# Kernel tuning notes

Hardware: AMD Instinct MI355X
Metric: run time of the kernel (lower is better)

## Reference

```python
import jax, jax.numpy as jnp
import numpy as np

B, S, D, H, O, E, K = 4, 2048, 1024, 2048, 1024, 8, 2

def setup_inputs() -> dict:
    key = jax.random.key(0)
    ks = jax.random.split(key, 8)
    x = jax.random.normal(ks[0], (B, S, D), dtype=jnp.float32)
    # kaiming-uniform-ish scale for weights, zero biases (as in _init_w)
    gate_w = jax.random.uniform(ks[1], (E, D), dtype=jnp.float32, minval=-1, maxval=1) * np.sqrt(6.0 / D)
    gate_b = jnp.zeros((E,), dtype=jnp.float32)
    w1 = jax.random.uniform(ks[2], (E, D, H), dtype=jnp.float32, minval=-1, maxval=1) * np.sqrt(6.0 / D)
    b1 = jnp.zeros((E, H), dtype=jnp.float32)
    w2 = jax.random.uniform(ks[3], (E, H, O), dtype=jnp.float32, minval=-1, maxval=1) * np.sqrt(6.0 / H)
    b2 = jnp.zeros((E, O), dtype=jnp.float32)
    return {"x": x, "gate_w": gate_w, "gate_b": gate_b, "w1": w1, "b1": b1, "w2": w2, "b2": b2}

def reference(x, gate_w, gate_b, w1, b1, w2, b2):
    # gate: softmax over experts, then top-k (k=2)
    logits = jnp.einsum('bsd,ed->bse', x, gate_w) + gate_b          # [B,S,E]
    probs = jax.nn.softmax(logits, axis=-1)
    topk_vals, topk_idx = jax.lax.top_k(probs, K)                    # [B,S,K]
    # dense all-expert MLPs (Linear-ReLU-Linear), dropout = 0
    h = jax.nn.relu(jnp.einsum('bsd,edh->bseh', x, w1) + b1)         # [B,S,E,H]
    expert_out = jnp.einsum('bseh,eho->bseo', h, w2) + b2            # [B,S,E,O]
    # gather top-k experts and combine with gate weights
    sel = jnp.take_along_axis(expert_out, topk_idx[..., None], axis=2)  # [B,S,K,O]
    return jnp.sum(sel * topk_vals[..., None], axis=2)               # [B,S,O]
```

## Files before the change

kernel.cpp:

```cpp
#include <hip/hip_runtime.h>

#define T_TOKENS 8192
#define D_DIM 1024
#define H_DIM 2048
#define O_DIM 1024
#define E_NUM 8
#define NPAIR 16384
#define GY_MAX 136

typedef unsigned short u16;
typedef __bf16 bf16x8 __attribute__((ext_vector_type(8)));
typedef float f32x4 __attribute__((ext_vector_type(4)));

#define VMCNT(n) asm volatile("s_waitcnt vmcnt(" #n ")" ::: "memory")

__device__ __forceinline__ void barsync() {
  asm volatile("" ::: "memory");
  __builtin_amdgcn_s_barrier();
  __builtin_amdgcn_sched_barrier(0);
}

__device__ inline u16 f2bf(float f) {
  union { float f; unsigned u; } v; v.f = f;
  unsigned r = v.u + 0x7FFFu + ((v.u >> 16) & 1u);
  return (u16)(r >> 16);
}

__device__ __forceinline__ void gload16(const u16* g, u16* l) {
  __builtin_amdgcn_global_load_lds((const __attribute__((address_space(1))) void*)g,
                                   (__attribute__((address_space(3))) void*)l, 16, 0, 0);
}

__global__ void transpose_cvt_kernel(const float* __restrict__ w, u16* __restrict__ wt,
                                     int R, int C) {
  __shared__ float tile[32][33];
  int e = blockIdx.z;
  int c0 = blockIdx.x * 32, r0 = blockIdx.y * 32;
  const float* wp = w + (size_t)e * R * C;
  u16* wtp = wt + (size_t)e * R * C;
  int tx = threadIdx.x, ty = threadIdx.y;
  #pragma unroll
  for (int j = 0; j < 32; j += 8)
    tile[ty + j][tx] = wp[(size_t)(r0 + ty + j) * C + c0 + tx];
  __syncthreads();
  #pragma unroll
  for (int j = 0; j < 32; j += 8)
    wtp[(size_t)(c0 + ty + j) * R + r0 + tx] = f2bf(tile[tx][ty + j]);
}

__global__ void gate_kernel(const float* __restrict__ x, const float* __restrict__ gw,
                            const float* __restrict__ gb, int* __restrict__ topk_idx,
                            float* __restrict__ topk_val, u16* __restrict__ xb) {
  int t = blockIdx.x * 4 + (threadIdx.x >> 6);
  int lane = threadIdx.x & 63;
  const float4* xr4 = (const float4*)(x + (size_t)t * D_DIM);
  const float4* gw4 = (const float4*)gw;
  u16* xbr = xb + (size_t)t * D_DIM;
  float acc[E_NUM];
  #pragma unroll
  for (int e = 0; e < E_NUM; e++) acc[e] = 0.f;
  #pragma unroll
  for (int it = 0; it < D_DIM / 256; ++it) {
    float4 xv = xr4[it * 64 + lane];
    ushort4 o;
    o.x = f2bf(xv.x); o.y = f2bf(xv.y); o.z = f2bf(xv.z); o.w = f2bf(xv.w);
    *(ushort4*)(xbr + (it * 64 + lane) * 4) = o;
    #pragma unroll
    for (int e = 0; e < E_NUM; e++) {
      float4 wv = gw4[e * (D_DIM / 4) + it * 64 + lane];
      acc[e] += xv.x * wv.x + xv.y * wv.y + xv.z * wv.z + xv.w * wv.w;
    }
  }
  #pragma unroll
  for (int e = 0; e < E_NUM; e++) {
    #pragma unroll
    for (int o = 32; o > 0; o >>= 1) acc[e] += __shfl_down(acc[e], o);
  }
  if (lane == 0) {
    float l[E_NUM], mx = -1e30f;
    #pragma unroll
    for (int e = 0; e < E_NUM; e++) { l[e] = acc[e] + gb[e]; mx = fmaxf(mx, l[e]); }
    float p[E_NUM], s = 0.f;
    #pragma unroll
    for (int e = 0; e < E_NUM; e++) { p[e] = expf(l[e] - mx); s += p[e]; }
    float inv = 1.f / s;
    int i1 = 0;
    #pragma unroll
    for (int e = 1; e < E_NUM; e++) if (p[e] > p[i1]) i1 = e;
    int i2 = (i1 == 0) ? 1 : 0;
    #pragma unroll
    for (int e = 0; e < E_NUM; e++) if (e != i1 && e != i2 && p[e] > p[i2]) i2 = e;
    topk_idx[t * 2] = i1;     topk_idx[t * 2 + 1] = i2;
    topk_val[t * 2] = p[i1] * inv; topk_val[t * 2 + 1] = p[i2] * inv;
  }
}

__global__ void histscan_kernel(const int* __restrict__ topk_idx,
                                int* __restrict__ counts, int* __restrict__ eoff,
                                int* __restrict__ nblk, int* __restrict__ tbl_e,
                                int* __restrict__ tbl_m0) {
  __shared__ int wh[4][E_NUM];
  int tid = threadIdx.x;
  int lane = tid & 63, wave = tid >> 6;
  int myc = 0;
  for (int i = tid; i < NPAIR; i += 256) {
    int e = topk_idx[i];
    #pragma unroll
    for (int ee = 0; ee < E_NUM; ee++) {
      unsigned long long m = __ballot(e == ee);
      if (lane == ee) myc += __popcll(m);
    }
  }
  if (lane < E_NUM) wh[wave][lane] = myc;
  __syncthreads();
  if (tid == 0) {
    int s = 0, cl[E_NUM];
    for (int e = 0; e < E_NUM; e++) {
      int c = wh[0][e] + wh[1][e] + wh[2][e] + wh[3][e];
      counts[e] = c;
      cl[e] = c;
      eoff[e] = s;
      s += c;
    }
    eoff[E_NUM] = s;
    int nb = 0;
    for (int e = 0; e < E_NUM; e++)
      for (int m0 = 0; m0 < cl[e]; m0 += 128) { tbl_e[nb] = e; tbl_m0[nb] = m0; nb++; }
    nblk[0] = nb;
  }
}

__global__ void scatter_kernel(const int* __restrict__ topk_idx, const float* __restrict__ topk_val,
                               const int* __restrict__ eoff, int* __restrict__ cursor_pad,
                               int* __restrict__ pair_token, float* __restrict__ pair_gate) {
  __shared__ int lhist[E_NUM];
  __shared__ int lbase[E_NUM];
  int tid = threadIdx.x;
  int t = blockIdx.x * 256 + tid;
  if (tid < E_NUM) lhist[tid] = 0;
  __syncthreads();
  int e0 = topk_idx[t * 2], e1 = topk_idx[t * 2 + 1];
  int r0 = atomicAdd(&lhist[e0], 1);
  int r1 = atomicAdd(&lhist[e1], 1);
  __syncthreads();
  if (tid < E_NUM) lbase[tid] = eoff[tid] + atomicAdd(&cursor_pad[tid * 32], lhist[tid]);
  __syncthreads();
  int p0 = lbase[e0] + r0;
  int p1 = lbase[e1] + r1;
  pair_token[p0] = t; pair_gate[p0] = topk_val[t * 2];
  pair_token[p1] = t; pair_gate[p1] = topk_val[t * 2 + 1];
}


#define GEMM_DECLS                                                             \
  __shared__ __align__(16) u16 As0[4096], Bs0[4096], As1[4096], Bs1[4096],     \
      As2[4096], Bs2[4096];                                                    \
  const int tid = threadIdx.x;                                                 \
  const int wid = tid >> 6;                                                    \
  const int lane = tid & 63;                                                   \
  const int wm = (wid & 1) * 64;                                               \
  const int wn = (wid >> 1) * 64;                                              \
  const int lrow = lane & 15;                                                  \
  const int quad = lane >> 4;                                                  \
  f32x4 acc[4][4] = {};                                                        \
  auto STAGE = [&](u16* Ab, u16* Bb, int k0) {                                 \
    _Pragma("unroll")                                                          \
    for (int j = 0; j < 2; j++) {                                              \
      gload16(aptrA[j] + k0, Ab + (wid * 16 + j * 8) * 64);                    \
      gload16(bptrB[j] + k0, Bb + (wid * 16 + j * 8) * 64);                    \
    }                                                                          \
  };                                                                           \
  auto COMPUTE = [&](const u16* Ab, const u16* Bb) {                           \
    bf16x8 af[4], bfr[4];                                                      \
    _Pragma("unroll")                                                          \
    for (int i = 0; i < 4; i++) {                                              \
      int r = wm + i * 16 + lrow;                                              \
      int p = r >> 1;                                                          \
      int s = (((r & 1) << 2) | quad) ^ (p & 7);                               \
      af[i] = *(const bf16x8*)&Ab[p * 64 + s * 8];                             \
    }                                                                          \
    _Pragma("unroll")                                                          \
    for (int j = 0; j < 4; j++) {                                              \
      int r = wn + j * 16 + lrow;                                              \
      int p = r >> 1;                                                          \
      int s = (((r & 1) << 2) | quad) ^ (p & 7);                               \
      bfr[j] = *(const bf16x8*)&Bb[p * 64 + s * 8];                            \
    }                                                                          \
    __builtin_amdgcn_s_setprio(1);                                             \
    _Pragma("unroll")                                                          \
    for (int i = 0; i < 4; i++)                                                \
      _Pragma("unroll")                                                        \
      for (int j = 0; j < 4; j++)                                              \
        acc[i][j] = __builtin_amdgcn_mfma_f32_16x16x32_bf16(af[i], bfr[j],     \
                                                            acc[i][j], 0, 0, 0);\
    __builtin_amdgcn_s_setprio(0);                                             \
  }

__global__ __launch_bounds__(256, 3) void gemm1_kernel(
    const u16* __restrict__ xb, const u16* __restrict__ w1t, const float* __restrict__ b1,
    const int* __restrict__ pair_token, const int* __restrict__ eoff,
    const int* __restrict__ ecnt, const int* __restrict__ nblk,
    const int* __restrict__ tbl_e, const int* __restrict__ tbl_m0,
    u16* __restrict__ hbuf) {
  int lin = blockIdx.y * 16 + blockIdx.x;
  int swz = (lin & 7) * (16 * GY_MAX / 8) + (lin >> 3);
  const int bx = swz & 15;
  const int yb = swz >> 4;
  if (yb >= nblk[0]) return;
  const int e = tbl_e[yb];
  const int m0t = tbl_m0[yb];
  const int ne = ecnt[e];
  const int off = eoff[e];
  const int n0 = bx * 128;

  const u16* aptrA[2]; const u16* bptrB[2];
  {
    const int wid_ = threadIdx.x >> 6, lane_ = threadIdx.x & 63;
    #pragma unroll
    for (int j = 0; j < 2; j++) {
      int p = wid_ * 16 + j * 8 + (lane_ >> 3);
      int u = (lane_ & 7) ^ (p & 7);
      int r = 2 * p + (u >> 2);
      int c = u & 3;
      int gm = m0t + r;
      int tok = (gm < ne) ? pair_token[off + gm] : 0;
      aptrA[j] = xb + (size_t)tok * D_DIM + c * 8;
      bptrB[j] = w1t + ((size_t)e * H_DIM + (n0 + r)) * D_DIM + c * 8;
    }
  }

  GEMM_DECLS;

  STAGE(As0, Bs0, 0); STAGE(As1, Bs1, 32); STAGE(As2, Bs2, 64);
  #pragma unroll 1
  for (int t = 0; t <= 32 - 6; t += 3) {
    VMCNT(8); barsync(); COMPUTE(As0, Bs0); barsync(); STAGE(As0, Bs0, (t + 3) * 32);
    VMCNT(8); barsync(); COMPUTE(As1, Bs1); barsync(); STAGE(As1, Bs1, (t + 4) * 32);
    VMCNT(8); barsync(); COMPUTE(As2, Bs2); barsync(); STAGE(As2, Bs2, (t + 5) * 32);
  }
  VMCNT(8); barsync(); COMPUTE(As0, Bs0); barsync(); STAGE(As0, Bs0, 30 * 32);
  VMCNT(8); barsync(); COMPUTE(As1, Bs1); barsync(); STAGE(As1, Bs1, 31 * 32);
  VMCNT(8); barsync(); COMPUTE(As2, Bs2);
  VMCNT(4); barsync(); COMPUTE(As0, Bs0);
  VMCNT(0); barsync(); COMPUTE(As1, Bs1);

  #pragma unroll
  for (int i = 0; i < 4; i++) {
    #pragma unroll
    for (int r = 0; r < 4; r++) {
      int m = wm + i * 16 + quad * 4 + r;
      int gm = m0t + m;
      if (gm >= ne) continue;
      size_t rowbase = (size_t)(off + gm) * H_DIM;
      #pragma unroll
      for (int j = 0; j < 4; j++) {
        int n = n0 + wn + j * 16 + lrow;
        float v = acc[i][j][r] + b1[e * H_DIM + n];
        v = v > 0.f ? v : 0.f;
        hbuf[rowbase + n] = f2bf(v);
      }
    }
  }
}

__global__ __launch_bounds__(256, 3) void gemm2_kernel(
    const u16* __restrict__ hbuf, const u16* __restrict__ w2t, const float* __restrict__ b2,
    const int* __restrict__ pair_token, const float* __restrict__ pair_gate,
    const int* __restrict__ eoff, const int* __restrict__ ecnt,
    const int* __restrict__ nblk, const int* __restrict__ tbl_e,
    const int* __restrict__ tbl_m0, float* __restrict__ out) {
  int lin = blockIdx.y * 8 + blockIdx.x;
  int swz = (lin & 7) * (8 * GY_MAX / 8) + (lin >> 3);
  const int bx = swz & 7;
  const int yb = swz >> 3;
  if (yb >= nblk[0]) return;
  const int e = tbl_e[yb];
  const int m0t = tbl_m0[yb];
  const int ne = ecnt[e];
  const int off = eoff[e];
  const int n0 = bx * 128;

  const u16* aptrA[2]; const u16* bptrB[2];
  {
    const int wid_ = threadIdx.x >> 6, lane_ = threadIdx.x & 63;
    #pragma unroll
    for (int j = 0; j < 2; j++) {
      int p = wid_ * 16 + j * 8 + (lane_ >> 3);
      int u = (lane_ & 7) ^ (p & 7);
      int r = 2 * p + (u >> 2);
      int c = u & 3;
      aptrA[j] = hbuf + (size_t)(off + m0t + r) * H_DIM + c * 8;
      bptrB[j] = w2t + ((size_t)e * O_DIM + (n0 + r)) * H_DIM + c * 8;
    }
  }

  GEMM_DECLS;

  STAGE(As0, Bs0, 0); STAGE(As1, Bs1, 32); STAGE(As2, Bs2, 64);
  #pragma unroll 1
  for (int t = 0; t <= 64 - 6; t += 3) {
    VMCNT(8); barsync(); COMPUTE(As0, Bs0); barsync(); STAGE(As0, Bs0, (t + 3) * 32);
    VMCNT(8); barsync(); COMPUTE(As1, Bs1); barsync(); STAGE(As1, Bs1, (t + 4) * 32);
    VMCNT(8); barsync(); COMPUTE(As2, Bs2); barsync(); STAGE(As2, Bs2, (t + 5) * 32);
  }
  VMCNT(8); barsync(); COMPUTE(As0, Bs0); barsync(); STAGE(As0, Bs0, 63 * 32);
  VMCNT(8); barsync(); COMPUTE(As1, Bs1);
  VMCNT(4); barsync(); COMPUTE(As2, Bs2);
  VMCNT(0); barsync(); COMPUTE(As0, Bs0);

  #pragma unroll
  for (int i = 0; i < 4; i++) {
    #pragma unroll
    for (int r = 0; r < 4; r++) {
      int m = wm + i * 16 + quad * 4 + r;
      int gm = m0t + m;
      if (gm >= ne) continue;
      int pair = off + gm;
      int tok = pair_token[pair];
      float g = pair_gate[pair];
      #pragma unroll
      for (int j = 0; j < 4; j++) {
        int n = n0 + wn + j * 16 + lrow;
        float v = (acc[i][j][r] + b2[e * O_DIM + n]) * g;
        atomicAdd(&out[(size_t)tok * O_DIM + n], v);
      }
    }
  }
}

extern "C" void kernel_launch(void* const* d_in, const int* in_sizes, int n_in,
                              void* d_out, int out_size, void* d_ws, size_t ws_size,
                              hipStream_t stream) {
  const float* x  = (const float*)d_in[0];
  const float* gw = (const float*)d_in[1];
  const float* gb = (const float*)d_in[2];
  const float* w1 = (const float*)d_in[3];
  const float* b1 = (const float*)d_in[4];
  const float* w2 = (const float*)d_in[5];
  const float* b2 = (const float*)d_in[6];
  float* out = (float*)d_out;

  char* ws = (char*)d_ws;
  size_t off = 0;
  auto take = [&](size_t bytes) -> char* {
    char* p = ws + off;
    off = (off + bytes + 255) & ~(size_t)255;
    return p;
  };
  int*   meta       = (int*)take(4096);
  int*   cursor_pad = meta;
  int*   counts     = meta + 256;
  int*   eoff       = meta + 264;
  int*   nblk       = meta + 273;
  int*   tbl_e      = meta + 274;
  int*   tbl_m0     = meta + 410;
  int*   topk_idx   = (int*)take((size_t)T_TOKENS * 2 * 4);
  float* topk_val   = (float*)take((size_t)T_TOKENS * 2 * 4);
  int*   pair_token = (int*)take((size_t)(NPAIR + 256) * 4);
  float* pair_gate  = (float*)take((size_t)(NPAIR + 256) * 4);
  u16*   xb         = (u16*)take((size_t)T_TOKENS * D_DIM * 2);
  u16*   w1t        = (u16*)take((size_t)E_NUM * D_DIM * H_DIM * 2);
  u16*   w2t        = (u16*)take((size_t)E_NUM * H_DIM * O_DIM * 2);
  u16*   hbuf       = (u16*)take((size_t)(NPAIR + 128) * H_DIM * 2);

  hipMemsetAsync(meta, 0, 4096, stream);
  hipMemsetAsync(out, 0, (size_t)T_TOKENS * O_DIM * 4, stream);

  transpose_cvt_kernel<<<dim3(H_DIM / 32, D_DIM / 32, E_NUM), dim3(32, 8), 0, stream>>>(w1, w1t, D_DIM, H_DIM);
  transpose_cvt_kernel<<<dim3(O_DIM / 32, H_DIM / 32, E_NUM), dim3(32, 8), 0, stream>>>(w2, w2t, H_DIM, O_DIM);
  gate_kernel<<<T_TOKENS / 4, 256, 0, stream>>>(x, gw, gb, topk_idx, topk_val, xb);
  histscan_kernel<<<1, 256, 0, stream>>>(topk_idx, counts, eoff, nblk, tbl_e, tbl_m0);
  scatter_kernel<<<T_TOKENS / 256, 256, 0, stream>>>(topk_idx, topk_val, eoff, cursor_pad, pair_token, pair_gate);
  gemm1_kernel<<<dim3(16, GY_MAX), 256, 0, stream>>>(xb, w1t, b1, pair_token, eoff, counts, nblk, tbl_e, tbl_m0, hbuf);
  gemm2_kernel<<<dim3(8, GY_MAX), 256, 0, stream>>>(hbuf, w2t, b2, pair_token, pair_gate, eoff, counts, nblk, tbl_e, tbl_m0, out);
}
```

Measured before the change: 505.3 us.

## Enlarge expert GEMM tiles to 256x256 with 512 threads and split-K in gemm2

Both grouped GEMMs move from 128x128 tiles with 256 threads and triple buffering to 256x256 tiles with 512 threads, 64-wide K steps and double buffering. LDS reads are issued as hand-written ds_read_b128 instructions, interleaved with staged global-to-LDS loads and explicit waitcnt and sched_barrier fences. Gemm2 splits K in two halves that are combined by the existing atomic adds, and the bias is added only by the first half. The larger tiles aim to raise arithmetic intensity and data reuse per block, at the cost of more padding waste per expert and doubled atomic traffic on the output.

```diff
diff --git a/kernel.cpp b/kernel.cpp
--- a/kernel.cpp
+++ b/kernel.cpp
@@ -6,18 +6,32 @@
 #define O_DIM 1024
 #define E_NUM 8
 #define NPAIR 16384
-#define GY_MAX 136
+#define GT_MAX 72
 
 typedef unsigned short u16;
 typedef __bf16 bf16x8 __attribute__((ext_vector_type(8)));
 typedef float f32x4 __attribute__((ext_vector_type(4)));
 
-#define VMCNT(n) asm volatile("s_waitcnt vmcnt(" #n ")" ::: "memory")
+#define VMC(IMM)                                                   \
+  __builtin_amdgcn_sched_barrier(0);                               \
+  asm volatile("s_waitcnt vmcnt(" #IMM ")" ::: "memory")
+#define LGKM0                                                      \
+  asm volatile("s_waitcnt lgkmcnt(0)" ::: "memory");               \
+  __builtin_amdgcn_sched_barrier(0)
+#define SB0 __builtin_amdgcn_sched_barrier(0)
 
 __device__ __forceinline__ void barsync() {
   asm volatile("" ::: "memory");
   __builtin_amdgcn_s_barrier();
   __builtin_amdgcn_sched_barrier(0);
+}
+
+#define DSR(dst, base, IMM)                                        \
+  asm volatile("ds_read_b128 %0, %1 offset:" #IMM                  \
+               : "=v"(dst) : "v"(base))
+
+__device__ __forceinline__ unsigned ldsaddr(const u16* p) {
+  return (unsigned)(size_t)(const __attribute__((address_space(3))) u16*)p;
 }
 
 __device__ inline u16 f2bf(float f) {
@@ -125,7 +139,7 @@
     eoff[E_NUM] = s;
     int nb = 0;
     for (int e = 0; e < E_NUM; e++)
-      for (int m0 = 0; m0 < cl[e]; m0 += 128) { tbl_e[nb] = e; tbl_m0[nb] = m0; nb++; }
+      for (int m0 = 0; m0 < cl[e]; m0 += 256) { tbl_e[nb] = e; tbl_m0[nb] = m0; nb++; }
     nblk[0] = nb;
   }
 }
@@ -152,125 +166,82 @@
 }
 
 
-#define GEMM_DECLS                                                             \
-  __shared__ __align__(16) u16 As0[4096], Bs0[4096], As1[4096], Bs1[4096],     \
-      As2[4096], Bs2[4096];                                                    \
-  const int tid = threadIdx.x;                                                 \
-  const int wid = tid >> 6;                                                    \
-  const int lane = tid & 63;                                                   \
-  const int wm = (wid & 1) * 64;                                               \
-  const int wn = (wid >> 1) * 64;                                              \
-  const int lrow = lane & 15;                                                  \
-  const int quad = lane >> 4;                                                  \
-  f32x4 acc[4][4] = {};                                                        \
-  auto STAGE = [&](u16* Ab, u16* Bb, int k0) {                                 \
-    _Pragma("unroll")                                                          \
-    for (int j = 0; j < 2; j++) {                                              \
-      gload16(aptrA[j] + k0, Ab + (wid * 16 + j * 8) * 64);                    \
-      gload16(bptrB[j] + k0, Bb + (wid * 16 + j * 8) * 64);                    \
-    }                                                                          \
-  };                                                                           \
-  auto COMPUTE = [&](const u16* Ab, const u16* Bb) {                           \
-    bf16x8 af[4], bfr[4];                                                      \
-    _Pragma("unroll")                                                          \
-    for (int i = 0; i < 4; i++) {                                              \
-      int r = wm + i * 16 + lrow;                                              \
-      int p = r >> 1;                                                          \
-      int s = (((r & 1) << 2) | quad) ^ (p & 7);                               \
-      af[i] = *(const bf16x8*)&Ab[p * 64 + s * 8];                             \
-    }                                                                          \
-    _Pragma("unroll")                                                          \
-    for (int j = 0; j < 4; j++) {                                              \
-      int r = wn + j * 16 + lrow;                                              \
-      int p = r >> 1;                                                          \
-      int s = (((r & 1) << 2) | quad) ^ (p & 7);                               \
-      bfr[j] = *(const bf16x8*)&Bb[p * 64 + s * 8];                            \
-    }                                                                          \
-    __builtin_amdgcn_s_setprio(1);                                             \
-    _Pragma("unroll")                                                          \
-    for (int i = 0; i < 4; i++)                                                \
-      _Pragma("unroll")                                                        \
-      for (int j = 0; j < 4; j++)                                              \
-        acc[i][j] = __builtin_amdgcn_mfma_f32_16x16x32_bf16(af[i], bfr[j],     \
-                                                            acc[i][j], 0, 0, 0);\
-    __builtin_amdgcn_s_setprio(0);                                             \
-  }
-
-__global__ __launch_bounds__(256, 3) void gemm1_kernel(
+#define MFMA16(I0)                                                              \
+  __builtin_amdgcn_s_setprio(1);                                                \
+  _Pragma("unroll")                                                             \
+  for (int j = 0; j < 4; ++j) {                                                 \
+    acc[I0][j]     = __builtin_amdgcn_mfma_f32_16x16x32_bf16(af[0][0], bf[j][0], acc[I0][j], 0, 0, 0);     \
+    acc[I0][j]     = __builtin_amdgcn_mfma_f32_16x16x32_bf16(af[0][1], bf[j][1], acc[I0][j], 0, 0, 0);     \
+    acc[I0 + 1][j] = __builtin_amdgcn_mfma_f32_16x16x32_bf16(af[1][0], bf[j][0], acc[I0 + 1][j], 0, 0, 0); \
+    acc[I0 + 1][j] = __builtin_amdgcn_mfma_f32_16x16x32_bf16(af[1][1], bf[j][1], acc[I0 + 1][j], 0, 0, 0); \
+  }                                                                             \
+  __builtin_amdgcn_s_setprio(0)
+
+#define READS_P0                                                                \
+  DSR(bf[0][0], bB0, 0); DSR(bf[1][0], bB0, 2048); DSR(bf[2][0], bB0, 4096); DSR(bf[3][0], bB0, 6144); \
+  DSR(bf[0][1], bB1, 0); DSR(bf[1][1], bB1, 2048); DSR(bf[2][1], bB1, 4096); DSR(bf[3][1], bB1, 6144); \
+  DSR(af[0][0], aA0, 0); DSR(af[1][0], aA0, 2048); DSR(af[0][1], aA1, 0); DSR(af[1][1], aA1, 2048)
+
+#define READS_AF(O0, O1)                                                        \
+  DSR(af[0][0], aA0, O0); DSR(af[1][0], aA0, O1);                               \
+  DSR(af[0][1], aA1, O0); DSR(af[1][1], aA1, O1)
+
+#define STAGE_A(ARR, H, K1)                                                     \
+  gload16(aptrA[H][0] + (K1), &ARR[(H) * 8192 + (wid * 16 + 0) * 64]);          \
+  gload16(aptrA[H][1] + (K1), &ARR[(H) * 8192 + (wid * 16 + 8) * 64])
+#define STAGE_B(ARR, H, K1)                                                     \
+  gload16(bptrB[H][0] + (K1), &ARR[(H) * 8192 + (wid * 16 + 0) * 64]);          \
+  gload16(bptrB[H][1] + (K1), &ARR[(H) * 8192 + (wid * 16 + 8) * 64])
+
+#define TILE(AcB, BcB, AN, BN, K1, VMIMM, DOSTAGE)                              \
+  {                                                                             \
+    unsigned aA0 = (AcB) + aoffs0, aA1 = (AcB) + aoffs1;                        \
+    unsigned bB0 = (BcB) + boffs0, bB1 = (BcB) + boffs1;                        \
+                                                                        \
+    if (DOSTAGE) { STAGE_A(AN, 0, K1); }                                        \
+    VMC(VMIMM);                                                                 \
+    barsync();                                                                  \
+    READS_P0; LGKM0; MFMA16(0); barsync();                                      \
+                                                                        \
+    READS_AF(4096, 6144);                                                       \
+    if (DOSTAGE) { STAGE_A(AN, 1, K1); } SB0;                                   \
+    barsync(); LGKM0; MFMA16(2); barsync();                                     \
+                                                                        \
+    READS_AF(8192, 10240);                                                      \
+    if (DOSTAGE) { STAGE_B(BN, 0, K1); } SB0;                                   \
+    barsync(); LGKM0; MFMA16(4); barsync();                                     \
+                                                                        \
+    READS_AF(12288, 14336);                                                     \
+    if (DOSTAGE) { STAGE_B(BN, 1, K1); } SB0;                                   \
+    barsync(); LGKM0; MFMA16(6); barsync();                                     \
+  }
+
+#define GEMM_CORE_DECLS                                                         \
+  __shared__ __align__(16) u16 A0s[16384], B0s[16384], A1s[16384], B1s[16384];  \
+  const int tid = threadIdx.x;                                                  \
+  const int wid = tid >> 6;                                                     \
+  const int lane = tid & 63;                                                    \
+  const int wm = wid & 1;                                                       \
+  const int wn = wid >> 1;                                                      \
+  const unsigned lrow = lane & 15;                                              \
+  const unsigned quad = lane >> 4;                                              \
+  const unsigned A0b = ldsaddr(A0s), B0b = ldsaddr(B0s);                        \
+  const unsigned A1b = ldsaddr(A1s), B1b = ldsaddr(B1s);                        \
+  const unsigned aoffs0 = ((wm * 128 + lrow) * 64 + ((quad ^ (lrow & 7)) * 8)) * 2;       \
+  const unsigned aoffs1 = ((wm * 128 + lrow) * 64 + (((4 + quad) ^ (lrow & 7)) * 8)) * 2; \
+  const unsigned boffs0 = ((wn * 64 + lrow) * 64 + ((quad ^ (lrow & 7)) * 8)) * 2;        \
+  const unsigned boffs1 = ((wn * 64 + lrow) * 64 + (((4 + quad) ^ (lrow & 7)) * 8)) * 2;  \
+  f32x4 acc[8][4] = {};                                                         \
+  bf16x8 af[2][2], bf[4][2];
+
+__global__ __launch_bounds__(512, 2) void gemm1_kernel(
     const u16* __restrict__ xb, const u16* __restrict__ w1t, const float* __restrict__ b1,
     const int* __restrict__ pair_token, const int* __restrict__ eoff,
     const int* __restrict__ ecnt, const int* __restrict__ nblk,
     const int* __restrict__ tbl_e, const int* __restrict__ tbl_m0,
     u16* __restrict__ hbuf) {
-  int lin = blockIdx.y * 16 + blockIdx.x;
-  int swz = (lin & 7) * (16 * GY_MAX / 8) + (lin >> 3);
-  const int bx = swz & 15;
-  const int yb = swz >> 4;
-  if (yb >= nblk[0]) return;
-  const int e = tbl_e[yb];
-  const int m0t = tbl_m0[yb];
-  const int ne = ecnt[e];
-  const int off = eoff[e];
-  const int n0 = bx * 128;
-
-  const u16* aptrA[2]; const u16* bptrB[2];
-  {
-    const int wid_ = threadIdx.x >> 6, lane_ = threadIdx.x & 63;
-    #pragma unroll
-    for (int j = 0; j < 2; j++) {
-      int p = wid_ * 16 + j * 8 + (lane_ >> 3);
-      int u = (lane_ & 7) ^ (p & 7);
-      int r = 2 * p + (u >> 2);
-      int c = u & 3;
-      int gm = m0t + r;
-      int tok = (gm < ne) ? pair_token[off + gm] : 0;
-      aptrA[j] = xb + (size_t)tok * D_DIM + c * 8;
-      bptrB[j] = w1t + ((size_t)e * H_DIM + (n0 + r)) * D_DIM + c * 8;
-    }
-  }
-
-  GEMM_DECLS;
-
-  STAGE(As0, Bs0, 0); STAGE(As1, Bs1, 32); STAGE(As2, Bs2, 64);
-  #pragma unroll 1
-  for (int t = 0; t <= 32 - 6; t += 3) {
-    VMCNT(8); barsync(); COMPUTE(As0, Bs0); barsync(); STAGE(As0, Bs0, (t + 3) * 32);
-    VMCNT(8); barsync(); COMPUTE(As1, Bs1); barsync(); STAGE(As1, Bs1, (t + 4) * 32);
-    VMCNT(8); barsync(); COMPUTE(As2, Bs2); barsync(); STAGE(As2, Bs2, (t + 5) * 32);
-  }
-  VMCNT(8); barsync(); COMPUTE(As0, Bs0); barsync(); STAGE(As0, Bs0, 30 * 32);
-  VMCNT(8); barsync(); COMPUTE(As1, Bs1); barsync(); STAGE(As1, Bs1, 31 * 32);
-  VMCNT(8); barsync(); COMPUTE(As2, Bs2);
-  VMCNT(4); barsync(); COMPUTE(As0, Bs0);
-  VMCNT(0); barsync(); COMPUTE(As1, Bs1);
-
-  #pragma unroll
-  for (int i = 0; i < 4; i++) {
-    #pragma unroll
-    for (int r = 0; r < 4; r++) {
-      int m = wm + i * 16 + quad * 4 + r;
-      int gm = m0t + m;
-      if (gm >= ne) continue;
-      size_t rowbase = (size_t)(off + gm) * H_DIM;
-      #pragma unroll
-      for (int j = 0; j < 4; j++) {
-        int n = n0 + wn + j * 16 + lrow;
-        float v = acc[i][j][r] + b1[e * H_DIM + n];
-        v = v > 0.f ? v : 0.f;
-        hbuf[rowbase + n] = f2bf(v);
-      }
-    }
-  }
-}
-
-__global__ __launch_bounds__(256, 3) void gemm2_kernel(
-    const u16* __restrict__ hbuf, const u16* __restrict__ w2t, const float* __restrict__ b2,
-    const int* __restrict__ pair_token, const float* __restrict__ pair_gate,
-    const int* __restrict__ eoff, const int* __restrict__ ecnt,
-    const int* __restrict__ nblk, const int* __restrict__ tbl_e,
-    const int* __restrict__ tbl_m0, float* __restrict__ out) {
-  int lin = blockIdx.y * 8 + blockIdx.x;
-  int swz = (lin & 7) * (8 * GY_MAX / 8) + (lin >> 3);
+  int lin = blockIdx.x;
+  int swz = (lin & 7) * (8 * GT_MAX / 8) + (lin >> 3);
   const int bx = swz & 7;
   const int yb = swz >> 3;
   if (yb >= nblk[0]) return;
@@ -278,41 +249,96 @@
   const int m0t = tbl_m0[yb];
   const int ne = ecnt[e];
   const int off = eoff[e];
-  const int n0 = bx * 128;
-
-  const u16* aptrA[2]; const u16* bptrB[2];
-  {
-    const int wid_ = threadIdx.x >> 6, lane_ = threadIdx.x & 63;
+  const int n0 = bx * 256;
+
+  GEMM_CORE_DECLS;
+
+  const u16* aptrA[2][2]; const u16* bptrB[2][2];
+  #pragma unroll
+  for (int h = 0; h < 2; h++)
     #pragma unroll
     for (int j = 0; j < 2; j++) {
-      int p = wid_ * 16 + j * 8 + (lane_ >> 3);
-      int u = (lane_ & 7) ^ (p & 7);
-      int r = 2 * p + (u >> 2);
-      int c = u & 3;
-      aptrA[j] = hbuf + (size_t)(off + m0t + r) * H_DIM + c * 8;
-      bptrB[j] = w2t + ((size_t)e * O_DIM + (n0 + r)) * H_DIM + c * 8;
-    }
-  }
-
-  GEMM_DECLS;
-
-  STAGE(As0, Bs0, 0); STAGE(As1, Bs1, 32); STAGE(As2, Bs2, 64);
+      int rw = h * 128 + wid * 16 + j * 8 + (lane >> 3);
+      int sl = (lane & 7) ^ (rw & 7);
+      int gm = m0t + rw;
+      int tok = (gm < ne) ? pair_token[off + gm] : 0;
+      aptrA[h][j] = xb + (size_t)tok * D_DIM + sl * 8;
+      bptrB[h][j] = w1t + ((size_t)e * H_DIM + (n0 + rw)) * D_DIM + sl * 8;
+    }
+
+  STAGE_A(A0s, 0, 0); STAGE_A(A0s, 1, 0); STAGE_B(B0s, 0, 0); STAGE_B(B0s, 1, 0);
   #pragma unroll 1
-  for (int t = 0; t <= 64 - 6; t += 3) {
-    VMCNT(8); barsync(); COMPUTE(As0, Bs0); barsync(); STAGE(As0, Bs0, (t + 3) * 32);
-    VMCNT(8); barsync(); COMPUTE(As1, Bs1); barsync(); STAGE(As1, Bs1, (t + 4) * 32);
-    VMCNT(8); barsync(); COMPUTE(As2, Bs2); barsync(); STAGE(As2, Bs2, (t + 5) * 32);
-  }
-  VMCNT(8); barsync(); COMPUTE(As0, Bs0); barsync(); STAGE(As0, Bs0, 63 * 32);
-  VMCNT(8); barsync(); COMPUTE(As1, Bs1);
-  VMCNT(4); barsync(); COMPUTE(As2, Bs2);
-  VMCNT(0); barsync(); COMPUTE(As0, Bs0);
-
-  #pragma unroll
-  for (int i = 0; i < 4; i++) {
+  for (int tt = 0; tt < 14; tt += 2) {
+    TILE(A0b, B0b, A1s, B1s, (tt + 1) * 64, 2, true);
+    TILE(A1b, B1b, A0s, B0s, (tt + 2) * 64, 2, true);
+  }
+  TILE(A0b, B0b, A1s, B1s, 15 * 64, 2, true);
+  TILE(A1b, B1b, A0s, B0s, 0, 0, false);
+
+  #pragma unroll
+  for (int i = 0; i < 8; i++) {
     #pragma unroll
     for (int r = 0; r < 4; r++) {
-      int m = wm + i * 16 + quad * 4 + r;
+      int m = wm * 128 + i * 16 + quad * 4 + r;
+      int gm = m0t + m;
+      if (gm >= ne) continue;
+      size_t rowbase = (size_t)(off + gm) * H_DIM;
+      #pragma unroll
+      for (int j = 0; j < 4; j++) {
+        int n = n0 + wn * 64 + j * 16 + lrow;
+        float v = acc[i][j][r] + b1[e * H_DIM + n];
+        v = v > 0.f ? v : 0.f;
+        hbuf[rowbase + n] = f2bf(v);
+      }
+    }
+  }
+}
+
+__global__ __launch_bounds__(512, 2) void gemm2_kernel(
+    const u16* __restrict__ hbuf, const u16* __restrict__ w2t, const float* __restrict__ b2,
+    const int* __restrict__ pair_token, const float* __restrict__ pair_gate,
+    const int* __restrict__ eoff, const int* __restrict__ ecnt,
+    const int* __restrict__ nblk, const int* __restrict__ tbl_e,
+    const int* __restrict__ tbl_m0, float* __restrict__ out) {
+  int lin = blockIdx.x;
+  int swz = (lin & 7) * (8 * GT_MAX / 8) + (lin >> 3);
+  const int bx = swz & 3;
+  const int ks = (swz >> 2) & 1;
+  const int yb = swz >> 3;
+  if (yb >= nblk[0]) return;
+  const int e = tbl_e[yb];
+  const int m0t = tbl_m0[yb];
+  const int ne = ecnt[e];
+  const int off = eoff[e];
+  const int n0 = bx * 256;
+
+  GEMM_CORE_DECLS;
+
+  const u16* aptrA[2][2]; const u16* bptrB[2][2];
+  #pragma unroll
+  for (int h = 0; h < 2; h++)
+    #pragma unroll
+    for (int j = 0; j < 2; j++) {
+      int rw = h * 128 + wid * 16 + j * 8 + (lane >> 3);
+      int sl = (lane & 7) ^ (rw & 7);
+      aptrA[h][j] = hbuf + (size_t)(off + m0t + rw) * H_DIM + ks * 1024 + sl * 8;
+      bptrB[h][j] = w2t + ((size_t)e * O_DIM + (n0 + rw)) * H_DIM + ks * 1024 + sl * 8;
+    }
+
+  STAGE_A(A0s, 0, 0); STAGE_A(A0s, 1, 0); STAGE_B(B0s, 0, 0); STAGE_B(B0s, 1, 0);
+  #pragma unroll 1
+  for (int tt = 0; tt < 14; tt += 2) {
+    TILE(A0b, B0b, A1s, B1s, (tt + 1) * 64, 2, true);
+    TILE(A1b, B1b, A0s, B0s, (tt + 2) * 64, 2, true);
+  }
+  TILE(A0b, B0b, A1s, B1s, 15 * 64, 2, true);
+  TILE(A1b, B1b, A0s, B0s, 0, 0, false);
+
+  #pragma unroll
+  for (int i = 0; i < 8; i++) {
+    #pragma unroll
+    for (int r = 0; r < 4; r++) {
+      int m = wm * 128 + i * 16 + quad * 4 + r;
       int gm = m0t + m;
       if (gm >= ne) continue;
       int pair = off + gm;
@@ -320,8 +346,8 @@
       float g = pair_gate[pair];
       #pragma unroll
       for (int j = 0; j < 4; j++) {
-        int n = n0 + wn + j * 16 + lrow;
-        float v = (acc[i][j][r] + b2[e * O_DIM + n]) * g;
+        int n = n0 + wn * 64 + j * 16 + lrow;
+        float v = (acc[i][j][r] + (ks ? 0.f : b2[e * O_DIM + n])) * g;
         atomicAdd(&out[(size_t)tok * O_DIM + n], v);
       }
     }
@@ -353,7 +379,7 @@
   int*   eoff       = meta + 264;
   int*   nblk       = meta + 273;
   int*   tbl_e      = meta + 274;
-  int*   tbl_m0     = meta + 410;
+  int*   tbl_m0     = meta + 346;
   int*   topk_idx   = (int*)take((size_t)T_TOKENS * 2 * 4);
   float* topk_val   = (float*)take((size_t)T_TOKENS * 2 * 4);
   int*   pair_token = (int*)take((size_t)(NPAIR + 256) * 4);
@@ -361,7 +387,7 @@
   u16*   xb         = (u16*)take((size_t)T_TOKENS * D_DIM * 2);
   u16*   w1t        = (u16*)take((size_t)E_NUM * D_DIM * H_DIM * 2);
   u16*   w2t        = (u16*)take((size_t)E_NUM * H_DIM * O_DIM * 2);
-  u16*   hbuf       = (u16*)take((size_t)(NPAIR + 128) * H_DIM * 2);
+  u16*   hbuf       = (u16*)take((size_t)(NPAIR + 256) * H_DIM * 2);
 
   hipMemsetAsync(meta, 0, 4096, stream);
   hipMemsetAsync(out, 0, (size_t)T_TOKENS * O_DIM * 4, stream);
@@ -371,6 +397,6 @@
   gate_kernel<<<T_TOKENS / 4, 256, 0, stream>>>(x, gw, gb, topk_idx, topk_val, xb);
   histscan_kernel<<<1, 256, 0, stream>>>(topk_idx, counts, eoff, nblk, tbl_e, tbl_m0);
   scatter_kernel<<<T_TOKENS / 256, 256, 0, stream>>>(topk_idx, topk_val, eoff, cursor_pad, pair_token, pair_gate);
-  gemm1_kernel<<<dim3(16, GY_MAX), 256, 0, stream>>>(xb, w1t, b1, pair_token, eoff, counts, nblk, tbl_e, tbl_m0, hbuf);
-  gemm2_kernel<<<dim3(8, GY_MAX), 256, 0, stream>>>(hbuf, w2t, b2, pair_token, pair_gate, eoff, counts, nblk, tbl_e, tbl_m0, out);
-}
+  gemm1_kernel<<<dim3(8 * GT_MAX), 512, 0, stream>>>(xb, w1t, b1, pair_token, eoff, counts, nblk, tbl_e, tbl_m0, hbuf);
+  gemm2_kernel<<<dim3(8 * GT_MAX), 512, 0, stream>>>(hbuf, w2t, b2, pair_token, pair_gate, eoff, counts, nblk, tbl_e, tbl_m0, out);
+}
```

After: 601.8 us. 19.1% more time.

## Replace atomic scatter-add in gemm2 with per-pair output buffer and combine kernel

Applied to the files above, without the earlier changes.

gemm2 now writes each pair's expert output (plus bias) to a dense fp32 buffer indexed by pair position instead of atomically adding gate-scaled results into the token output. A new combine kernel reads each token's two pair rows through an inverse position map and writes the gated sum directly, which also removes the memset of the output. This trades the scattered atomic traffic for an extra 64MB write and read of the intermediate buffer plus one more kernel launch.

```diff
diff --git a/kernel.cpp b/kernel.cpp
--- a/kernel.cpp
+++ b/kernel.cpp
@@ -132,7 +132,7 @@
 
 __global__ void scatter_kernel(const int* __restrict__ topk_idx, const float* __restrict__ topk_val,
                                const int* __restrict__ eoff, int* __restrict__ cursor_pad,
-                               int* __restrict__ pair_token, float* __restrict__ pair_gate) {
+                               int* __restrict__ pair_token, int* __restrict__ inv_pos) {
   __shared__ int lhist[E_NUM];
   __shared__ int lbase[E_NUM];
   int tid = threadIdx.x;
@@ -147,8 +147,27 @@
   __syncthreads();
   int p0 = lbase[e0] + r0;
   int p1 = lbase[e1] + r1;
-  pair_token[p0] = t; pair_gate[p0] = topk_val[t * 2];
-  pair_token[p1] = t; pair_gate[p1] = topk_val[t * 2 + 1];
+  pair_token[p0] = t;
+  pair_token[p1] = t;
+  inv_pos[t * 2] = p0;
+  inv_pos[t * 2 + 1] = p1;
+}
+
+__global__ void combine_kernel(const float* __restrict__ obuf, const int* __restrict__ inv_pos,
+                               const float* __restrict__ topk_val, float* __restrict__ out) {
+  int t = blockIdx.x;
+  int tid = threadIdx.x;
+  int p0 = inv_pos[t * 2], p1 = inv_pos[t * 2 + 1];
+  float g0 = topk_val[t * 2], g1 = topk_val[t * 2 + 1];
+  const float4* a4 = (const float4*)(obuf + (size_t)p0 * O_DIM);
+  const float4* b4 = (const float4*)(obuf + (size_t)p1 * O_DIM);
+  float4 a = a4[tid], b = b4[tid];
+  float4 r;
+  r.x = g0 * a.x + g1 * b.x;
+  r.y = g0 * a.y + g1 * b.y;
+  r.z = g0 * a.z + g1 * b.z;
+  r.w = g0 * a.w + g1 * b.w;
+  ((float4*)(out + (size_t)t * O_DIM))[tid] = r;
 }
 
 
@@ -265,10 +284,9 @@
 
 __global__ __launch_bounds__(256, 3) void gemm2_kernel(
     const u16* __restrict__ hbuf, const u16* __restrict__ w2t, const float* __restrict__ b2,
-    const int* __restrict__ pair_token, const float* __restrict__ pair_gate,
     const int* __restrict__ eoff, const int* __restrict__ ecnt,
     const int* __restrict__ nblk, const int* __restrict__ tbl_e,
-    const int* __restrict__ tbl_m0, float* __restrict__ out) {
+    const int* __restrict__ tbl_m0, float* __restrict__ obuf) {
   int lin = blockIdx.y * 8 + blockIdx.x;
   int swz = (lin & 7) * (8 * GY_MAX / 8) + (lin >> 3);
   const int bx = swz & 7;
@@ -315,14 +333,11 @@
       int m = wm + i * 16 + quad * 4 + r;
       int gm = m0t + m;
       if (gm >= ne) continue;
-      int pair = off + gm;
-      int tok = pair_token[pair];
-      float g = pair_gate[pair];
+      size_t rowbase = (size_t)(off + gm) * O_DIM;
       #pragma unroll
       for (int j = 0; j < 4; j++) {
         int n = n0 + wn + j * 16 + lrow;
-        float v = (acc[i][j][r] + b2[e * O_DIM + n]) * g;
-        atomicAdd(&out[(size_t)tok * O_DIM + n], v);
+        obuf[rowbase + n] = acc[i][j][r] + b2[e * O_DIM + n];
       }
     }
   }
@@ -357,20 +372,21 @@
   int*   topk_idx   = (int*)take((size_t)T_TOKENS * 2 * 4);
   float* topk_val   = (float*)take((size_t)T_TOKENS * 2 * 4);
   int*   pair_token = (int*)take((size_t)(NPAIR + 256) * 4);
-  float* pair_gate  = (float*)take((size_t)(NPAIR + 256) * 4);
+  int*   inv_pos    = (int*)take((size_t)T_TOKENS * 2 * 4);
   u16*   xb         = (u16*)take((size_t)T_TOKENS * D_DIM * 2);
   u16*   w1t        = (u16*)take((size_t)E_NUM * D_DIM * H_DIM * 2);
   u16*   w2t        = (u16*)take((size_t)E_NUM * H_DIM * O_DIM * 2);
   u16*   hbuf       = (u16*)take((size_t)(NPAIR + 128) * H_DIM * 2);
+  float* obuf       = (float*)take((size_t)(NPAIR + 128) * O_DIM * 4);
 
   hipMemsetAsync(meta, 0, 4096, stream);
-  hipMemsetAsync(out, 0, (size_t)T_TOKENS * O_DIM * 4, stream);
 
   transpose_cvt_kernel<<<dim3(H_DIM / 32, D_DIM / 32, E_NUM), dim3(32, 8), 0, stream>>>(w1, w1t, D_DIM, H_DIM);
   transpose_cvt_kernel<<<dim3(O_DIM / 32, H_DIM / 32, E_NUM), dim3(32, 8), 0, stream>>>(w2, w2t, H_DIM, O_DIM);
   gate_kernel<<<T_TOKENS / 4, 256, 0, stream>>>(x, gw, gb, topk_idx, topk_val, xb);
   histscan_kernel<<<1, 256, 0, stream>>>(topk_idx, counts, eoff, nblk, tbl_e, tbl_m0);
-  scatter_kernel<<<T_TOKENS / 256, 256, 0, stream>>>(topk_idx, topk_val, eoff, cursor_pad, pair_token, pair_gate);
+  scatter_kernel<<<T_TOKENS / 256, 256, 0, stream>>>(topk_idx, topk_val, eoff, cursor_pad, pair_token, inv_pos);
   gemm1_kernel<<<dim3(16, GY_MAX), 256, 0, stream>>>(xb, w1t, b1, pair_token, eoff, counts, nblk, tbl_e, tbl_m0, hbuf);
-  gemm2_kernel<<<dim3(8, GY_MAX), 256, 0, stream>>>(hbuf, w2t, b2, pair_token, pair_gate, eoff, counts, nblk, tbl_e, tbl_m0, out);
-}
+  gemm2_kernel<<<dim3(8, GY_MAX), 256, 0, stream>>>(hbuf, w2t, b2, eoff, counts, nblk, tbl_e, tbl_m0, obuf);
+  combine_kernel<<<T_TOKENS, 256, 0, stream>>>(obuf, inv_pos, topk_val, out);
+}
```

New measurement: 451.5 us. -10.6%, faster.
